# Kernel optimization log

Measured on AMD Instinct MI355X. Metric: run time of the kernel, lower is better.

## Reference

```python
import jax, jax.numpy as jnp
import numpy as np

N, E = 50000, 640000
D_IN, D_OUT, N_BASES = 128, 128, 8


def setup_inputs() -> dict:
    key = jax.random.key(0)
    k1, k2, k3, k4, k5, k6 = jax.random.split(key, 6)
    x = jax.random.normal(k1, (N, D_IN), dtype=jnp.float32)
    edge_index = jax.random.randint(k2, (2, E), 0, N, dtype=jnp.int64)
    # basis-decomposed relation weights (num_relations=1)
    bases = jax.random.normal(k3, (N_BASES, D_IN, D_OUT), dtype=jnp.float32) * 0.05
    comp = jax.random.normal(k4, (1, N_BASES), dtype=jnp.float32)
    root = jax.random.normal(k5, (D_IN, D_OUT), dtype=jnp.float32) * 0.05
    bias = jax.random.normal(k6, (D_OUT,), dtype=jnp.float32) * 0.01
    return {"x": x, "edge_index": edge_index, "bases": bases,
            "comp": comp, "root": root, "bias": bias}


def reference(x, edge_index, bases, comp, root, bias):
    # W[rel=0] = sum_b comp[0,b] * bases[b]  -> [D_IN, D_OUT]
    W = jnp.einsum('b,bio->io', comp[0], bases)
    src = edge_index[0]  # message sources (x_j)
    dst = edge_index[1]  # aggregation targets
    # gather -> scatter-add (aggr='add'), then relation-specific transform
    agg = jax.ops.segment_sum(x[src], dst, num_segments=x.shape[0])  # [N, D_IN]
    out = agg @ W + x @ root + bias  # root/self-loop transform + bias
    return out
```

## Files before the change

kernel.cpp:

```cpp
#include <hip/hip_runtime.h>

#define N_NODES 50000
#define N_EDGES 640000
#define D 128
#define NB 8
#define PAD 32
#define BM 64

typedef _Float16 half_t;
typedef __attribute__((ext_vector_type(8))) _Float16 half8;
typedef __attribute__((ext_vector_type(4))) float f32x4;

__global__ __launch_bounds__(256)
void init_kernel(const float* __restrict__ bases,
                 const float* __restrict__ comp,
                 const float* __restrict__ root,
                 half_t* __restrict__ Wt,
                 half_t* __restrict__ Rt,
                 int* __restrict__ cnt) {
    int i = blockIdx.x * 256 + threadIdx.x;
    if (i < N_NODES) cnt[i] = 0;
    if (i < D * D) {
        int ii = i >> 7, o = i & 127;
        float acc = 0.f;
#pragma unroll
        for (int b = 0; b < NB; ++b)
            acc += comp[b] * bases[((size_t)b * D + ii) * D + o];
        Wt[o * D + ii] = (half_t)acc;
        Rt[o * D + ii] = (half_t)root[i];
    }
}

__global__ __launch_bounds__(256)
void gemm_kernel(const float* __restrict__ x,
                 const half_t* __restrict__ Wt,
                 const half_t* __restrict__ Rt,
                 const float* __restrict__ bias,
                 half_t* __restrict__ y,
                 float* __restrict__ out) {
    const int tid  = threadIdx.x;
    const int wave = tid >> 6;
    const int lane = tid & 63;
    const int m    = lane & 15;
    const int quad = lane >> 4;
    const int row0 = blockIdx.x * BM;
    const int arow = row0 + wave * 16 + m;

    const float4* x4 = (const float4*)x;
    size_t abase = (size_t)(arow < N_NODES ? arow : 0) * 32 + quad * 2;
    float4 xa[8];
#pragma unroll
    for (int kk = 0; kk < 4; ++kk) {
        xa[2 * kk]     = x4[abase + kk * 8];
        xa[2 * kk + 1] = x4[abase + kk * 8 + 1];
    }
    half8 a[4];
#pragma unroll
    for (int kk = 0; kk < 4; ++kk) {
        float4 v0 = xa[2 * kk], v1 = xa[2 * kk + 1];
        half8 h;
        h[0] = (half_t)v0.x; h[1] = (half_t)v0.y; h[2] = (half_t)v0.z; h[3] = (half_t)v0.w;
        h[4] = (half_t)v1.x; h[5] = (half_t)v1.y; h[6] = (half_t)v1.z; h[7] = (half_t)v1.w;
        a[kk] = h;
    }

    f32x4 accW[8], accR[8];
#pragma unroll
    for (int nt = 0; nt < 8; ++nt) {
        accW[nt] = (f32x4){0.f, 0.f, 0.f, 0.f};
        accR[nt] = (f32x4){0.f, 0.f, 0.f, 0.f};
    }
#pragma unroll
    for (int nt = 0; nt < 8; ++nt) {
        const half_t* wp = Wt + (nt * 16 + m) * D + quad * 8;
        const half_t* rp = Rt + (nt * 16 + m) * D + quad * 8;
        half8 bw[4], br[4];
#pragma unroll
        for (int kk = 0; kk < 4; ++kk) {
            bw[kk] = *(const half8*)(wp + kk * 32);
            br[kk] = *(const half8*)(rp + kk * 32);
        }
#pragma unroll
        for (int kk = 0; kk < 4; ++kk) {
            accW[nt] = __builtin_amdgcn_mfma_f32_16x16x32_f16(a[kk], bw[kk], accW[nt], 0, 0, 0);
            accR[nt] = __builtin_amdgcn_mfma_f32_16x16x32_f16(a[kk], br[kk], accR[nt], 0, 0, 0);
        }
    }
#pragma unroll
    for (int nt = 0; nt < 8; ++nt) {
        int col = nt * 16 + m;
        float bb = bias[col];
#pragma unroll
        for (int r = 0; r < 4; ++r) {
            int row = row0 + wave * 16 + quad * 4 + r;
            if (row < N_NODES) {
                y[(size_t)row * D + col]   = (half_t)accW[nt][r];
                out[(size_t)row * D + col] = accR[nt][r] + bb;
            }
        }
    }
}

__global__ __launch_bounds__(256)
void bucket_kernel(const int* __restrict__ eidx,
                   const half_t* __restrict__ y,
                   float* __restrict__ out,
                   int* __restrict__ cnt,
                   int* __restrict__ bucket) {
    int e = blockIdx.x * 256 + threadIdx.x;
    if (e >= N_EDGES) return;
    int src = eidx[e];
    int dst = eidx[N_EDGES + e];
    int pos = atomicAdd(&cnt[dst], 1);
    if (pos < PAD) {
        bucket[(size_t)dst * PAD + pos] = src;
    } else {
        const half_t* yr = y + (size_t)src * D;
        float* op = out + (size_t)dst * D;
        for (int q = 0; q < D; ++q) atomicAdd(op + q, (float)yr[q]);
    }
}

__global__ __launch_bounds__(256)
void gather_kernel(const int* __restrict__ cnt,
                   const int* __restrict__ bucket,
                   const half_t* __restrict__ y,
                   float* __restrict__ out) {
    int node = blockIdx.x * 16 + (threadIdx.x >> 4);
    int q = threadIdx.x & 15;
    if (node >= N_NODES) return;
    int c = cnt[node];
    if (c > PAD) c = PAD;
    const int* b = bucket + (size_t)node * PAD;
    float acc[8] = {0.f, 0.f, 0.f, 0.f, 0.f, 0.f, 0.f, 0.f};
    int i = 0;
    for (; i + 8 <= c; i += 8) {
        int4 s0 = *(const int4*)(b + i);
        int4 s1 = *(const int4*)(b + i + 4);
        half8 v0 = *(const half8*)(y + (size_t)s0.x * D + q * 8);
        half8 v1 = *(const half8*)(y + (size_t)s0.y * D + q * 8);
        half8 v2 = *(const half8*)(y + (size_t)s0.z * D + q * 8);
        half8 v3 = *(const half8*)(y + (size_t)s0.w * D + q * 8);
        half8 v4 = *(const half8*)(y + (size_t)s1.x * D + q * 8);
        half8 v5 = *(const half8*)(y + (size_t)s1.y * D + q * 8);
        half8 v6 = *(const half8*)(y + (size_t)s1.z * D + q * 8);
        half8 v7 = *(const half8*)(y + (size_t)s1.w * D + q * 8);
#pragma unroll
        for (int j = 0; j < 8; ++j)
            acc[j] += ((float)v0[j] + (float)v1[j]) + ((float)v2[j] + (float)v3[j])
                    + ((float)v4[j] + (float)v5[j]) + ((float)v6[j] + (float)v7[j]);
    }
    for (; i + 4 <= c; i += 4) {
        int4 s = *(const int4*)(b + i);
        half8 v0 = *(const half8*)(y + (size_t)s.x * D + q * 8);
        half8 v1 = *(const half8*)(y + (size_t)s.y * D + q * 8);
        half8 v2 = *(const half8*)(y + (size_t)s.z * D + q * 8);
        half8 v3 = *(const half8*)(y + (size_t)s.w * D + q * 8);
#pragma unroll
        for (int j = 0; j < 8; ++j)
            acc[j] += ((float)v0[j] + (float)v1[j]) + ((float)v2[j] + (float)v3[j]);
    }
    for (; i < c; ++i) {
        half8 v = *(const half8*)(y + (size_t)b[i] * D + q * 8);
#pragma unroll
        for (int j = 0; j < 8; ++j) acc[j] += (float)v[j];
    }
    float4* op = (float4*)(out + (size_t)node * D + q * 8);
    float4 o0 = op[0], o1 = op[1];
    o0.x += acc[0]; o0.y += acc[1]; o0.z += acc[2]; o0.w += acc[3];
    o1.x += acc[4]; o1.y += acc[5]; o1.z += acc[6]; o1.w += acc[7];
    op[0] = o0; op[1] = o1;
}

extern "C" void kernel_launch(void* const* d_in, const int* in_sizes, int n_in,
                              void* d_out, int out_size, void* d_ws, size_t ws_size,
                              hipStream_t stream) {
    const float* x     = (const float*)d_in[0];
    const int*   eidx  = (const int*)d_in[1];
    const float* bases = (const float*)d_in[2];
    const float* comp  = (const float*)d_in[3];
    const float* root  = (const float*)d_in[4];
    const float* bias  = (const float*)d_in[5];
    float* out = (float*)d_out;

    char* ws = (char*)d_ws;
    half_t* y      = (half_t*)ws;
    half_t* Wt     = (half_t*)(ws + 12800000);
    half_t* Rt     = (half_t*)(ws + 12832768);
    int*    cnt    = (int*)   (ws + 12865536);
    int*    bucket = (int*)   (ws + 13065536);

    init_kernel<<<(N_NODES + 255) / 256, 256, 0, stream>>>(
        bases, comp, root, Wt, Rt, cnt);
    gemm_kernel<<<(N_NODES + BM - 1) / BM, 256, 0, stream>>>(
        x, Wt, Rt, bias, y, out);
    bucket_kernel<<<(N_EDGES + 255) / 256, 256, 0, stream>>>(
        eidx, y, out, cnt, bucket);
    gather_kernel<<<(N_NODES + 15) / 16, 256, 0, stream>>>(
        cnt, bucket, y, out);
}
```

Measured before the change: 181.9 us.

## Make GEMM persistent with per-wave column slices and register-resident weights

The GEMM kernel becomes a persistent grid of 1024 blocks. Each wave owns a fixed 32-column slice of W and root, loads those weight fragments into registers once, and then strides over 16-row strips. Before, every wave reloaded all 128 columns of both weight matrices, so the goal is to cut that repeated weight traffic and register pressure, which allows an occupancy hint of 4. In exchange, each x row is now loaded and converted by four different waves, so x reads rise about fourfold. Output writes per wave become narrower column chunks.

```diff
diff --git a/kernel.cpp b/kernel.cpp
--- a/kernel.cpp
+++ b/kernel.cpp
@@ -5,7 +5,8 @@
 #define D 128
 #define NB 8
 #define PAD 32
-#define BM 64
+#define NSTRIP 3125
+#define GRID_G 1024
 
 typedef _Float16 half_t;
 typedef __attribute__((ext_vector_type(8))) _Float16 half8;
@@ -31,7 +32,7 @@
     }
 }
 
-__global__ __launch_bounds__(256)
+__global__ __launch_bounds__(256, 4)
 void gemm_kernel(const float* __restrict__ x,
                  const half_t* __restrict__ Wt,
                  const half_t* __restrict__ Rt,
@@ -43,59 +44,62 @@
     const int lane = tid & 63;
     const int m    = lane & 15;
     const int quad = lane >> 4;
-    const int row0 = blockIdx.x * BM;
-    const int arow = row0 + wave * 16 + m;
-
-    const float4* x4 = (const float4*)x;
-    size_t abase = (size_t)(arow < N_NODES ? arow : 0) * 32 + quad * 2;
-    float4 xa[8];
-#pragma unroll
-    for (int kk = 0; kk < 4; ++kk) {
-        xa[2 * kk]     = x4[abase + kk * 8];
-        xa[2 * kk + 1] = x4[abase + kk * 8 + 1];
-    }
-    half8 a[4];
-#pragma unroll
-    for (int kk = 0; kk < 4; ++kk) {
-        float4 v0 = xa[2 * kk], v1 = xa[2 * kk + 1];
-        half8 h;
-        h[0] = (half_t)v0.x; h[1] = (half_t)v0.y; h[2] = (half_t)v0.z; h[3] = (half_t)v0.w;
-        h[4] = (half_t)v1.x; h[5] = (half_t)v1.y; h[6] = (half_t)v1.z; h[7] = (half_t)v1.w;
-        a[kk] = h;
-    }
-
-    f32x4 accW[8], accR[8];
-#pragma unroll
-    for (int nt = 0; nt < 8; ++nt) {
-        accW[nt] = (f32x4){0.f, 0.f, 0.f, 0.f};
-        accR[nt] = (f32x4){0.f, 0.f, 0.f, 0.f};
-    }
-#pragma unroll
-    for (int nt = 0; nt < 8; ++nt) {
+    const int gw   = blockIdx.x * 4 + wave;
+    const int q    = gw & 3;
+    const int s0   = gw >> 2;
+    const int SSTR = GRID_G;
+
+    half8 bw[2][4], br[2][4];
+    float bb[2];
+#pragma unroll
+    for (int t = 0; t < 2; ++t) {
+        const int nt = 2 * q + t;
         const half_t* wp = Wt + (nt * 16 + m) * D + quad * 8;
         const half_t* rp = Rt + (nt * 16 + m) * D + quad * 8;
-        half8 bw[4], br[4];
 #pragma unroll
         for (int kk = 0; kk < 4; ++kk) {
-            bw[kk] = *(const half8*)(wp + kk * 32);
-            br[kk] = *(const half8*)(rp + kk * 32);
-        }
+            bw[t][kk] = *(const half8*)(wp + kk * 32);
+            br[t][kk] = *(const half8*)(rp + kk * 32);
+        }
+        bb[t] = bias[nt * 16 + m];
+    }
+
+    const float4* x4 = (const float4*)x;
+    for (int s = s0; s < NSTRIP; s += SSTR) {
+        size_t ab = (size_t)(s * 16 + m) * 32 + quad * 2;
+        half8 a[4];
 #pragma unroll
         for (int kk = 0; kk < 4; ++kk) {
-            accW[nt] = __builtin_amdgcn_mfma_f32_16x16x32_f16(a[kk], bw[kk], accW[nt], 0, 0, 0);
-            accR[nt] = __builtin_amdgcn_mfma_f32_16x16x32_f16(a[kk], br[kk], accR[nt], 0, 0, 0);
-        }
-    }
-#pragma unroll
-    for (int nt = 0; nt < 8; ++nt) {
-        int col = nt * 16 + m;
-        float bb = bias[col];
-#pragma unroll
-        for (int r = 0; r < 4; ++r) {
-            int row = row0 + wave * 16 + quad * 4 + r;
-            if (row < N_NODES) {
-                y[(size_t)row * D + col]   = (half_t)accW[nt][r];
-                out[(size_t)row * D + col] = accR[nt][r] + bb;
+            float4 v0 = x4[ab + kk * 8];
+            float4 v1 = x4[ab + kk * 8 + 1];
+            half8 h;
+            h[0] = (half_t)v0.x; h[1] = (half_t)v0.y; h[2] = (half_t)v0.z; h[3] = (half_t)v0.w;
+            h[4] = (half_t)v1.x; h[5] = (half_t)v1.y; h[6] = (half_t)v1.z; h[7] = (half_t)v1.w;
+            a[kk] = h;
+        }
+
+        f32x4 accW[2], accR[2];
+#pragma unroll
+        for (int t = 0; t < 2; ++t) {
+            accW[t] = (f32x4){0.f, 0.f, 0.f, 0.f};
+            accR[t] = (f32x4){0.f, 0.f, 0.f, 0.f};
+        }
+#pragma unroll
+        for (int t = 0; t < 2; ++t)
+#pragma unroll
+            for (int kk = 0; kk < 4; ++kk) {
+                accW[t] = __builtin_amdgcn_mfma_f32_16x16x32_f16(a[kk], bw[t][kk], accW[t], 0, 0, 0);
+                accR[t] = __builtin_amdgcn_mfma_f32_16x16x32_f16(a[kk], br[t][kk], accR[t], 0, 0, 0);
+            }
+
+#pragma unroll
+        for (int t = 0; t < 2; ++t) {
+            int col = (2 * q + t) * 16 + m;
+#pragma unroll
+            for (int r = 0; r < 4; ++r) {
+                int row = s * 16 + quad * 4 + r;
+                y[(size_t)row * D + col]   = (half_t)accW[t][r];
+                out[(size_t)row * D + col] = accR[t][r] + bb[t];
             }
         }
     }
@@ -192,7 +196,7 @@
 
     init_kernel<<<(N_NODES + 255) / 256, 256, 0, stream>>>(
         bases, comp, root, Wt, Rt, cnt);
-    gemm_kernel<<<(N_NODES + BM - 1) / BM, 256, 0, stream>>>(
+    gemm_kernel<<<GRID_G, 256, 0, stream>>>(
         x, Wt, Rt, bias, y, out);
     bucket_kernel<<<(N_EDGES + 255) / 256, 256, 0, stream>>>(
         eidx, y, out, cnt, bucket);
```

Result: faster. 167.9 us (-7.7%).
